# Performance work log

Measured on AMD Instinct MI355X. Metric: run time of the kernel, lower is better.

## Reference

```python
import jax, jax.numpy as jnp
import numpy as np

NUM_HEADS = 12


def setup_inputs() -> dict:
    key = jax.random.key(0)
    k1, k2, k3, k4, k5 = jax.random.split(key, 5)
    B, N, C = 64, 197, 768
    P = 10  # prefix length
    H, D = NUM_HEADS, C // NUM_HEADS
    return {
        "x": jax.random.normal(k1, (B, N, C), dtype=jnp.float32),
        "prompt": jax.random.normal(k2, (B, 2, P, H, D), dtype=jnp.float32),
        "qkv_w": jax.random.normal(k3, (3 * C, C), dtype=jnp.float32) * 0.02,
        "proj_w": jax.random.normal(k4, (C, C), dtype=jnp.float32) * 0.02,
        "proj_b": jax.random.normal(k5, (C,), dtype=jnp.float32) * 0.02,
    }


def reference(x, prompt, qkv_w, proj_w, proj_b):
    B, N, C = x.shape
    H = NUM_HEADS
    D = C // H
    scale = D ** -0.5

    # qkv projection (no bias), split into per-head q, k, v: [B, H, N, D]
    qkv = jnp.einsum("bnc,fc->bnf", x, qkv_w)              # [B, N, 3C]
    qkv = qkv.reshape(B, N, 3, H, D).transpose(2, 0, 3, 1, 4)
    q, k, v = qkv[0], qkv[1], qkv[2]

    # prompt: [B, 2, P, H, D] -> [2, B, H, P, D]; concat prefix onto k, v
    p = prompt.transpose(1, 0, 3, 2, 4)
    k = jnp.concatenate([p[0], k], axis=2)                  # [B, H, P+N, D]
    v = jnp.concatenate([p[1], v], axis=2)

    attn = jnp.einsum("bhnd,bhmd->bhnm", q, k) * scale      # [B, H, N, P+N]
    attn = jax.nn.softmax(attn, axis=-1)                    # attn_drop p=0 -> identity

    out = jnp.einsum("bhnm,bhmd->bhnd", attn, v)            # [B, H, N, D]
    out = out.transpose(0, 2, 1, 3).reshape(B, N, C)
    out = jnp.einsum("bnc,oc->bno", out, proj_w) + proj_b   # proj_drop p=0 -> identity
    return out
```

## Files before the change

### kernel.cpp

```cpp
#include <hip/hip_runtime.h>
#include <hip/hip_bf16.h>
#include <stdint.h>

#define NH 12
#define DH 64
#define CC 768
#define NTOK 197
#define PFX 10
#define MKV 207
#define BB 64
#define MROWS (BB * NTOK)
#define MPAD (99 * 128)
#define NT_QKV 9
#define MT_QKV 50
#define MPAD2 (MT_QKV * 256)
#define KV_PAD 208
#define KV_PAD2 224

typedef __attribute__((__ext_vector_type__(8))) short bf16x8;
typedef __attribute__((__ext_vector_type__(4))) float f32x4;

__device__ __forceinline__ ushort f2bf(float f) {
    union { float f; uint32_t u; } x; x.f = f;
    uint32_t u = x.u;
    return (ushort)((u + 0x7fffu + ((u >> 16) & 1u)) >> 16);
}

__device__ __forceinline__ void gload_lds16(const void* g, void* l) {
    __builtin_amdgcn_global_load_lds(
        (const __attribute__((address_space(1))) void*)g,
        (__attribute__((address_space(3))) void*)l, 16, 0, 0);
}

__device__ __forceinline__ int xcd_chunked(int orig, int nwg) {
    int q = nwg >> 3, r = nwg & 7;
    int xcd = orig & 7, rem = orig >> 3;
    return (xcd < r ? xcd * (q + 1) : r * (q + 1) + (xcd - r) * q) + rem;
}

__global__ void cvt_bf16(const float* __restrict__ src, ushort* __restrict__ dst, int n4) {
    int i = blockIdx.x * 256 + threadIdx.x;
    if (i >= n4) return;
    float4 v = reinterpret_cast<const float4*>(src)[i];
    ushort4 o = make_ushort4(f2bf(v.x), f2bf(v.y), f2bf(v.z), f2bf(v.w));
    reinterpret_cast<ushort4*>(dst)[i] = o;
}

__global__ void prompt_scatter(const float* __restrict__ prompt,
                               ushort* __restrict__ kbuf, ushort* __restrict__ vt) {
    int i = blockIdx.x * 256 + threadIdx.x;
    if (i >= BB * 2 * PFX * NH * DH) return;
    int d = i & 63;
    int h = (i >> 6) % NH;
    int p = (i / (64 * NH)) % PFX;
    int s = (i / (64 * NH * PFX)) & 1;
    int b = i / (64 * NH * PFX * 2);
    ushort val = f2bf(prompt[i]);
    int bh = b * NH + h;
    if (s == 0) kbuf[(bh * KV_PAD + p) * DH + d] = val;
    else        vt[(bh * DH + d) * KV_PAD2 + p] = val;
}


#define STAGE6(kt) {                                                              \
    const int bsel = (kt) & 1; const int koff = (kt) * 64;                        \
    gload_lds16(pA[0] + koff, &lds[bsel][0][0 * 4096 + w * 512]);                 \
    gload_lds16(pA[2] + koff, &lds[bsel][0][2 * 4096 + w * 512]);                 \
    gload_lds16(pB[0] + koff, &lds[bsel][1][0 * 4096 + w * 512]);                 \
    gload_lds16(pB[1] + koff, &lds[bsel][1][1 * 4096 + w * 512]);                 \
    gload_lds16(pB[2] + koff, &lds[bsel][1][2 * 4096 + w * 512]);                 \
    gload_lds16(pB[3] + koff, &lds[bsel][1][3 * 4096 + w * 512]); }

#define STAGE2(kt) {                                                              \
    const int bsel = (kt) & 1; const int koff = (kt) * 64;                        \
    gload_lds16(pA[1] + koff, &lds[bsel][0][1 * 4096 + w * 512]);                 \
    gload_lds16(pA[3] + koff, &lds[bsel][0][3 * 4096 + w * 512]); }

#define PHASE(t, p, VMSTR, DOSTAGE) {                                             \
    if (DOSTAGE) { if ((p) == 0) STAGE6((t) + 1) else STAGE2((t) + 1) }           \
    asm volatile("s_waitcnt vmcnt(" VMSTR ")" ::: "memory");                      \
    __builtin_amdgcn_s_barrier();                                                 \
    __builtin_amdgcn_sched_barrier(0);                                            \
    const ushort* Ab = &lds[(t) & 1][0][0];                                       \
    const ushort* Bb = &lds[(t) & 1][1][0];                                       \
    bf16x8 af[4][2], bf[4][2];                                                    \
    _Pragma("unroll") for (int i = 0; i < 4; ++i)                                 \
      _Pragma("unroll") for (int ks = 0; ks < 2; ++ks)                            \
        af[i][ks] = *reinterpret_cast<const bf16x8*>(                             \
            &Ab[(wm * 128 + ((p) * 4 + i) * 16 + lr) * 64 + coff[ks]]);           \
    _Pragma("unroll") for (int n = 0; n < 4; ++n)                                 \
      _Pragma("unroll") for (int ks = 0; ks < 2; ++ks)                            \
        bf[n][ks] = *reinterpret_cast<const bf16x8*>(                             \
            &Bb[(wn * 64 + n * 16 + lr) * 64 + coff[ks]]);                        \
    __builtin_amdgcn_s_setprio(1);                                                \
    _Pragma("unroll") for (int ks = 0; ks < 2; ++ks)                              \
      _Pragma("unroll") for (int i = 0; i < 4; ++i)                               \
        _Pragma("unroll") for (int n = 0; n < 4; ++n)                             \
          acc[(p) * 4 + i][n] = __builtin_amdgcn_mfma_f32_16x16x32_bf16(          \
              af[i][ks], bf[n][ks], acc[(p) * 4 + i][n], 0, 0, 0);                \
    __builtin_amdgcn_s_setprio(0);                                                \
    __builtin_amdgcn_s_barrier();                                                 \
    __builtin_amdgcn_sched_barrier(0);                                            \
}

__global__ __launch_bounds__(512, 2) void gemm_qkv8(const ushort* __restrict__ A,
                                                    const ushort* __restrict__ Bw,
                                                    ushort* __restrict__ qbuf,
                                                    ushort* __restrict__ kbuf,
                                                    ushort* __restrict__ vt) {
    __shared__ __align__(16) ushort lds[2][2][256 * 64];
    const int tid  = threadIdx.x;
    const int lane = tid & 63;
    const int w    = tid >> 6;
    const int wm = w >> 2, wn = w & 3;
    const int g = lane >> 4, lr = lane & 15;
    const int wgid = xcd_chunked(blockIdx.x, gridDim.x);
    const int row0 = (wgid / NT_QKV) * 256;
    const int col0 = (wgid % NT_QKV) * 256;

    const int sr  = tid >> 3;
    const int scb = (((tid & 7) ^ ((tid >> 3) & 7)) << 3);
    const int lr7 = lr & 7;
    int coff[2];
    coff[0] = ((0 * 4 + g) ^ lr7) << 3;
    coff[1] = ((1 * 4 + g) ^ lr7) << 3;

    const ushort* pA[4];
    #pragma unroll
    for (int q = 0; q < 4; ++q)
        pA[q] = A + (size_t)(row0 + q * 64 + sr) * CC + scb;
    const ushort* pB[4];
    #pragma unroll
    for (int j = 0; j < 4; ++j)
        pB[j] = Bw + (size_t)(col0 + j * 64 + sr) * CC + scb;

    f32x4 acc[8][4] = {};

    STAGE6(0)
    STAGE2(0)

    for (int t = 0; t < 11; ++t) {
        PHASE(t, 0, "8", true)
        PHASE(t, 1, "8", true)
    }
    PHASE(11, 0, "2", false)
    PHASE(11, 1, "0", false)

    #pragma unroll
    for (int ni = 0; ni < 4; ++ni) {
        int f = col0 + wn * 64 + ni * 16 + lr;
        int s   = f / CC;
        int rem = f - s * CC;
        int h = rem >> 6, d = rem & 63;
        #pragma unroll
        for (int mi = 0; mi < 8; ++mi) {
            #pragma unroll
            for (int rr = 0; rr < 4; ++rr) {
                int r = row0 + wm * 128 + mi * 16 + g * 4 + rr;
                if (r >= MROWS) continue;
                int b = r / NTOK;
                int n = r - b * NTOK;
                ushort val = f2bf(acc[mi][ni][rr]);
                int bh = b * NH + h;
                if (s == 0)      qbuf[(bh * KV_PAD + n) * DH + d] = val;
                else if (s == 1) kbuf[(bh * KV_PAD + n + PFX) * DH + d] = val;
                else             vt[(bh * DH + d) * KV_PAD2 + n + PFX] = val;
            }
        }
    }
}

#define GEMM_PRE(A_, B_, KDIM, NTILES)                                               \
    __shared__ __align__(16) ushort Alds0[128 * 32];                                 \
    __shared__ __align__(16) ushort Blds0[128 * 32];                                 \
    __shared__ __align__(16) ushort Alds1[128 * 32];                                 \
    __shared__ __align__(16) ushort Blds1[128 * 32];                                 \
    const int tid  = threadIdx.x;                                                    \
    const int lane = tid & 63;                                                       \
    const int wave = tid >> 6;                                                       \
    const int wm = wave >> 1, wn = wave & 1;                                         \
    const int g = lane >> 4, lr = lane & 15;                                         \
    const int wgid = xcd_chunked(blockIdx.x, gridDim.x);                             \
    const int row0 = (wgid / (NTILES)) * 128;                                        \
    const int col0 = (wgid % (NTILES)) * 128;                                        \
    const int srow = lane >> 2;                                                      \
    const int scol = (lane & 3) * 8;                                                 \
    const ushort* gA0 = &(A_)[(size_t)(row0 + wave * 16 + srow) * (KDIM) + scol];    \
    const ushort* gA1 = gA0 + (size_t)64 * (KDIM);                                   \
    const ushort* gB0 = &(B_)[(size_t)(col0 + wave * 16 + srow) * (KDIM) + scol];    \
    const ushort* gB1 = gB0 + (size_t)64 * (KDIM);                                   \
    f32x4 acc[4][4] = {};

#define GEMM_STAGE(AB, BB_, KOFF)                                                    \
    gload_lds16(gA0 + (KOFF), &(AB)[(wave * 16) * 32]);                              \
    gload_lds16(gA1 + (KOFF), &(AB)[(64 + wave * 16) * 32]);                         \
    gload_lds16(gB0 + (KOFF), &(BB_)[(wave * 16) * 32]);                             \
    gload_lds16(gB1 + (KOFF), &(BB_)[(64 + wave * 16) * 32]);

#define GEMM_COMPUTE(AB, BB_)                                                        \
    {                                                                                \
        bf16x8 af[4], bfr[4];                                                        \
        _Pragma("unroll")                                                            \
        for (int i = 0; i < 4; ++i)                                                  \
            af[i] = *reinterpret_cast<const bf16x8*>(&(AB)[(wm * 64 + i * 16 + lr) * 32 + g * 8]); \
        _Pragma("unroll")                                                            \
        for (int i = 0; i < 4; ++i)                                                  \
            bfr[i] = *reinterpret_cast<const bf16x8*>(&(BB_)[(wn * 64 + i * 16 + lr) * 32 + g * 8]); \
        _Pragma("unroll")                                                            \
        for (int mi = 0; mi < 4; ++mi)                                               \
            _Pragma("unroll")                                                        \
            for (int ni = 0; ni < 4; ++ni)                                           \
                acc[mi][ni] = __builtin_amdgcn_mfma_f32_16x16x32_bf16(af[mi], bfr[ni], acc[mi][ni], 0, 0, 0); \
    }

#define GEMM_MAIN(A_, B_, KDIM, NTILES)                                              \
    GEMM_PRE(A_, B_, KDIM, NTILES)                                                   \
    GEMM_STAGE(Alds0, Blds0, 0)                                                      \
    __syncthreads();                                                                 \
    for (int k0 = 0; k0 < (KDIM); k0 += 64) {                                        \
        GEMM_STAGE(Alds1, Blds1, k0 + 32)                                            \
        GEMM_COMPUTE(Alds0, Blds0)                                                   \
        __syncthreads();                                                             \
        if (k0 + 64 < (KDIM)) { GEMM_STAGE(Alds0, Blds0, k0 + 64) }                  \
        GEMM_COMPUTE(Alds1, Blds1)                                                   \
        __syncthreads();                                                             \
    }

__global__ __launch_bounds__(256) void gemm_proj(const ushort* __restrict__ A,
                                                 const ushort* __restrict__ Bw,
                                                 const float* __restrict__ bias,
                                                 float* __restrict__ out) {
    GEMM_MAIN(A, Bw, CC, 6)
    #pragma unroll
    for (int ni = 0; ni < 4; ++ni) {
        int o = col0 + wn * 64 + ni * 16 + lr;
        float bs = bias[o];
        #pragma unroll
        for (int mi = 0; mi < 4; ++mi) {
            #pragma unroll
            for (int rr = 0; rr < 4; ++rr) {
                int r = row0 + wm * 64 + mi * 16 + g * 4 + rr;
                if (r >= MROWS) continue;
                out[(size_t)r * CC + o] = acc[mi][ni][rr] + bs;
            }
        }
    }
}

__global__ __launch_bounds__(64) void attn(const ushort* __restrict__ qbuf,
                                           const ushort* __restrict__ kbuf,
                                           const ushort* __restrict__ vt,
                                           ushort* __restrict__ aout) {
    __shared__ __align__(16) ushort Plds[16][232];
    const int lane = threadIdx.x;
    const int g = lane >> 4, lr = lane & 15;
    const int wgid = xcd_chunked(blockIdx.x, gridDim.x);
    const int bh = wgid / 13;
    const int qt = wgid % 13;
    const int b = bh / NH;
    const int h = bh - b * NH;
    const ushort* Q  = qbuf + (size_t)bh * KV_PAD * DH;
    const ushort* Kb = kbuf + (size_t)bh * KV_PAD * DH;
    const ushort* V  = vt   + (size_t)bh * DH * KV_PAD2;

    bf16x8 qf[2];
    #pragma unroll
    for (int kc = 0; kc < 2; ++kc)
        qf[kc] = *reinterpret_cast<const bf16x8*>(&Q[(qt * 16 + lr) * DH + kc * 32 + g * 8]);

    f32x4 s[13];
    __builtin_amdgcn_s_setprio(1);
    #pragma unroll
    for (int t = 0; t < 13; ++t) {
        f32x4 a = {};
        #pragma unroll
        for (int kc = 0; kc < 2; ++kc) {
            bf16x8 kf = *reinterpret_cast<const bf16x8*>(&Kb[(t * 16 + lr) * DH + kc * 32 + g * 8]);
            a = __builtin_amdgcn_mfma_f32_16x16x32_bf16(kf, qf[kc], a, 0, 0, 0);
        }
        s[t] = a;
    }
    __builtin_amdgcn_s_setprio(0);

    float m = -1e30f;
    #pragma unroll
    for (int t = 0; t < 13; ++t) {
        #pragma unroll
        for (int rr = 0; rr < 4; ++rr) {
            int kv = t * 16 + g * 4 + rr;
            float v = (kv < MKV) ? s[t][rr] : -1e30f;
            s[t][rr] = v;
            m = fmaxf(m, v);
        }
    }
    m = fmaxf(m, __shfl_xor(m, 16));
    m = fmaxf(m, __shfl_xor(m, 32));

    const float cs = 0.125f * 1.4426950408889634f;
    float sum = 0.f;
    #pragma unroll
    for (int t = 0; t < 13; ++t) {
        #pragma unroll
        for (int rr = 0; rr < 4; ++rr) {
            float p = exp2f((s[t][rr] - m) * cs);
            s[t][rr] = p;
            sum += p;
        }
    }
    sum += __shfl_xor(sum, 16);
    sum += __shfl_xor(sum, 32);
    float inv = 1.0f / sum;

    {
        int row = lane >> 2;
        int col = 208 + (lane & 3) * 4;
        *reinterpret_cast<ushort4*>(&Plds[row][col]) = make_ushort4(0, 0, 0, 0);
    }
    #pragma unroll
    for (int t = 0; t < 13; ++t) {
        #pragma unroll
        for (int rr = 0; rr < 4; ++rr)
            Plds[lr][t * 16 + g * 4 + rr] = f2bf(s[t][rr] * inv);
    }
    __syncthreads();

    const int q = qt * 16 + lr;
    #pragma unroll
    for (int dt = 0; dt < 4; ++dt) {
        f32x4 o = {};
        __builtin_amdgcn_s_setprio(1);
        #pragma unroll
        for (int kc = 0; kc < 7; ++kc) {
            bf16x8 vf = *reinterpret_cast<const bf16x8*>(&V[(dt * 16 + lr) * KV_PAD2 + kc * 32 + g * 8]);
            bf16x8 pf = *reinterpret_cast<const bf16x8*>(&Plds[lr][kc * 32 + g * 8]);
            o = __builtin_amdgcn_mfma_f32_16x16x32_bf16(vf, pf, o, 0, 0, 0);
        }
        __builtin_amdgcn_s_setprio(0);
        if (q < NTOK) {
            ushort4 st = make_ushort4(f2bf(o[0]), f2bf(o[1]), f2bf(o[2]), f2bf(o[3]));
            int r = b * NTOK + q;
            *reinterpret_cast<ushort4*>(&aout[(size_t)r * CC + h * 64 + dt * 16 + g * 4]) = st;
        }
    }
}

extern "C" void kernel_launch(void* const* d_in, const int* in_sizes, int n_in,
                              void* d_out, int out_size, void* d_ws, size_t ws_size,
                              hipStream_t stream) {
    const float* x      = (const float*)d_in[0];
    const float* prompt = (const float*)d_in[1];
    const float* qkv_w  = (const float*)d_in[2];
    const float* proj_w = (const float*)d_in[3];
    const float* proj_b = (const float*)d_in[4];
    float* out = (float*)d_out;

    char* ws = (char*)d_ws;
    ushort* Xb = (ushort*)(ws + 0);
    ushort* Wq = (ushort*)(ws + 19660800);
    ushort* Wp = (ushort*)(ws + 23199744);
    ushort* qb = (ushort*)(ws + 24379392);
    ushort* kb = (ushort*)(ws + 44826624);
    ushort* vt = (ushort*)(ws + 65273856);
    ushort* ao = (ushort*)(ws + 87293952);

    cvt_bf16<<<dim3((MROWS * CC / 4 + 255) / 256), 256, 0, stream>>>(x, Xb, MROWS * CC / 4);
    cvt_bf16<<<dim3((3 * CC * CC / 4 + 255) / 256), 256, 0, stream>>>(qkv_w, Wq, 3 * CC * CC / 4);
    cvt_bf16<<<dim3((CC * CC / 4 + 255) / 256), 256, 0, stream>>>(proj_w, Wp, CC * CC / 4);
    prompt_scatter<<<dim3((BB * 2 * PFX * NH * DH + 255) / 256), 256, 0, stream>>>(prompt, kb, vt);

    gemm_qkv8<<<dim3(MT_QKV * NT_QKV), 512, 0, stream>>>(Xb, Wq, qb, kb, vt);
    attn<<<dim3(13 * BB * NH), 64, 0, stream>>>(qb, kb, vt, ao);
    gemm_proj<<<dim3(99 * 6), 256, 0, stream>>>(ao, Wp, proj_b, out);
}
```

Baseline: 298.2 us.

## Process all query tiles of a head per block with K/V staged in LDS

Replaces the per-query-tile attention kernel with one workgroup per (batch, head) whose eight waves share K and V loaded once into LDS (K with an XOR swizzle, V with a padded stride). This removes the 13-fold redundant global/L2 reads of K and V across query tiles. Large LDS use limits occupancy, and waves 0-4 process two query tiles while others process one, creating imbalance.

```diff
diff --git a/kernel.cpp b/kernel.cpp
--- a/kernel.cpp
+++ b/kernel.cpp
@@ -16,6 +16,7 @@
 #define MPAD2 (MT_QKV * 256)
 #define KV_PAD 208
 #define KV_PAD2 224
+#define VSTRIDE 232
 
 typedef __attribute__((__ext_vector_type__(8))) short bf16x8;
 typedef __attribute__((__ext_vector_type__(4))) float f32x4;
@@ -60,7 +61,6 @@
     if (s == 0) kbuf[(bh * KV_PAD + p) * DH + d] = val;
     else        vt[(bh * DH + d) * KV_PAD2 + p] = val;
 }
-
 
 #define STAGE6(kt) {                                                              \
     const int bsel = (kt) & 1; const int koff = (kt) * 64;                        \
@@ -247,101 +247,135 @@
     }
 }
 
-__global__ __launch_bounds__(64) void attn(const ushort* __restrict__ qbuf,
-                                           const ushort* __restrict__ kbuf,
-                                           const ushort* __restrict__ vt,
-                                           ushort* __restrict__ aout) {
-    __shared__ __align__(16) ushort Plds[16][232];
-    const int lane = threadIdx.x;
+__global__ __launch_bounds__(512, 2) void attn_bh(const ushort* __restrict__ qbuf,
+                                                  const ushort* __restrict__ kbuf,
+                                                  const ushort* __restrict__ vt,
+                                                  ushort* __restrict__ aout) {
+    __shared__ __align__(16) ushort Klds[KV_PAD * DH];
+    __shared__ __align__(16) ushort Vlds[DH * VSTRIDE];
+    __shared__ __align__(16) ushort Plds[8 * 16 * VSTRIDE];
+    const int tid  = threadIdx.x;
+    const int lane = tid & 63;
+    const int w    = tid >> 6;
     const int g = lane >> 4, lr = lane & 15;
-    const int wgid = xcd_chunked(blockIdx.x, gridDim.x);
-    const int bh = wgid / 13;
-    const int qt = wgid % 13;
-    const int b = bh / NH;
-    const int h = bh - b * NH;
-    const ushort* Q  = qbuf + (size_t)bh * KV_PAD * DH;
-    const ushort* Kb = kbuf + (size_t)bh * KV_PAD * DH;
-    const ushort* V  = vt   + (size_t)bh * DH * KV_PAD2;
-
-    bf16x8 qf[2];
+    const int bh = blockIdx.x;
+    const int b = bh / NH, h = bh - b * NH;
+
+    const ushort* pKsrc = kbuf + (size_t)bh * KV_PAD * DH
+                        + (lane >> 3) * DH + (((lane & 7) ^ (lane >> 3)) << 3);
+    #pragma unroll
+    for (int u = 0; u < 4; ++u) {
+        int uu = w + u * 8;
+        if (uu < 26) gload_lds16(pKsrc + uu * 512, &Klds[uu * 512]);
+    }
+
+    const int4* vsrc = reinterpret_cast<const int4*>(vt + (size_t)bh * DH * KV_PAD2);
+    #pragma unroll
+    for (int k = 0; k < 4; ++k) {
+        int u = tid + 512 * k;
+        if (u < DH * (KV_PAD2 / 8)) {
+            int4 d = vsrc[u];
+            int row  = u / (KV_PAD2 / 8);
+            int colu = u - row * (KV_PAD2 / 8);
+            *reinterpret_cast<int4*>(&Vlds[row * VSTRIDE + colu * 8]) = d;
+        }
+    }
+
+    const ushort* Q = qbuf + (size_t)bh * KV_PAD * DH;
+    const int qt0 = w, qt1 = w + 8;
+    bf16x8 qf0[2], qf1[2];
     #pragma unroll
     for (int kc = 0; kc < 2; ++kc)
-        qf[kc] = *reinterpret_cast<const bf16x8*>(&Q[(qt * 16 + lr) * DH + kc * 32 + g * 8]);
-
-    f32x4 s[13];
-    __builtin_amdgcn_s_setprio(1);
-    #pragma unroll
-    for (int t = 0; t < 13; ++t) {
-        f32x4 a = {};
-        #pragma unroll
-        for (int kc = 0; kc < 2; ++kc) {
-            bf16x8 kf = *reinterpret_cast<const bf16x8*>(&Kb[(t * 16 + lr) * DH + kc * 32 + g * 8]);
-            a = __builtin_amdgcn_mfma_f32_16x16x32_bf16(kf, qf[kc], a, 0, 0, 0);
-        }
-        s[t] = a;
-    }
-    __builtin_amdgcn_s_setprio(0);
-
-    float m = -1e30f;
-    #pragma unroll
-    for (int t = 0; t < 13; ++t) {
-        #pragma unroll
-        for (int rr = 0; rr < 4; ++rr) {
-            int kv = t * 16 + g * 4 + rr;
-            float v = (kv < MKV) ? s[t][rr] : -1e30f;
-            s[t][rr] = v;
-            m = fmaxf(m, v);
-        }
-    }
-    m = fmaxf(m, __shfl_xor(m, 16));
-    m = fmaxf(m, __shfl_xor(m, 32));
-
+        qf0[kc] = *reinterpret_cast<const bf16x8*>(&Q[(qt0 * 16 + lr) * DH + kc * 32 + g * 8]);
+    if (qt1 < 13) {
+        #pragma unroll
+        for (int kc = 0; kc < 2; ++kc)
+            qf1[kc] = *reinterpret_cast<const bf16x8*>(&Q[(qt1 * 16 + lr) * DH + kc * 32 + g * 8]);
+    }
+
+    __syncthreads();
+
+    ushort* Pw = &Plds[w * 16 * VSTRIDE];
+    {
+        int row = lane >> 2, col = 208 + (lane & 3) * 4;
+        *reinterpret_cast<ushort4*>(&Pw[row * VSTRIDE + col]) = make_ushort4(0, 0, 0, 0);
+    }
+
+    const int kswz0 = ((0 * 4 + g) ^ (lr & 7)) << 3;
+    const int kswz1 = ((1 * 4 + g) ^ (lr & 7)) << 3;
     const float cs = 0.125f * 1.4426950408889634f;
-    float sum = 0.f;
-    #pragma unroll
-    for (int t = 0; t < 13; ++t) {
-        #pragma unroll
-        for (int rr = 0; rr < 4; ++rr) {
-            float p = exp2f((s[t][rr] - m) * cs);
-            s[t][rr] = p;
-            sum += p;
-        }
-    }
-    sum += __shfl_xor(sum, 16);
-    sum += __shfl_xor(sum, 32);
-    float inv = 1.0f / sum;
-
-    {
-        int row = lane >> 2;
-        int col = 208 + (lane & 3) * 4;
-        *reinterpret_cast<ushort4*>(&Plds[row][col]) = make_ushort4(0, 0, 0, 0);
-    }
-    #pragma unroll
-    for (int t = 0; t < 13; ++t) {
-        #pragma unroll
-        for (int rr = 0; rr < 4; ++rr)
-            Plds[lr][t * 16 + g * 4 + rr] = f2bf(s[t][rr] * inv);
-    }
-    __syncthreads();
-
-    const int q = qt * 16 + lr;
-    #pragma unroll
-    for (int dt = 0; dt < 4; ++dt) {
-        f32x4 o = {};
+
+    auto process = [&](int qt, bf16x8 qfa, bf16x8 qfb) {
+        f32x4 s[13];
         __builtin_amdgcn_s_setprio(1);
         #pragma unroll
-        for (int kc = 0; kc < 7; ++kc) {
-            bf16x8 vf = *reinterpret_cast<const bf16x8*>(&V[(dt * 16 + lr) * KV_PAD2 + kc * 32 + g * 8]);
-            bf16x8 pf = *reinterpret_cast<const bf16x8*>(&Plds[lr][kc * 32 + g * 8]);
-            o = __builtin_amdgcn_mfma_f32_16x16x32_bf16(vf, pf, o, 0, 0, 0);
+        for (int t = 0; t < 13; ++t) {
+            f32x4 a = {};
+            bf16x8 kf0 = *reinterpret_cast<const bf16x8*>(&Klds[(t * 16 + lr) * DH + kswz0]);
+            a = __builtin_amdgcn_mfma_f32_16x16x32_bf16(kf0, qfa, a, 0, 0, 0);
+            bf16x8 kf1 = *reinterpret_cast<const bf16x8*>(&Klds[(t * 16 + lr) * DH + kswz1]);
+            a = __builtin_amdgcn_mfma_f32_16x16x32_bf16(kf1, qfb, a, 0, 0, 0);
+            s[t] = a;
         }
         __builtin_amdgcn_s_setprio(0);
-        if (q < NTOK) {
-            ushort4 st = make_ushort4(f2bf(o[0]), f2bf(o[1]), f2bf(o[2]), f2bf(o[3]));
-            int r = b * NTOK + q;
-            *reinterpret_cast<ushort4*>(&aout[(size_t)r * CC + h * 64 + dt * 16 + g * 4]) = st;
-        }
-    }
+
+        float m = -1e30f;
+        #pragma unroll
+        for (int t = 0; t < 13; ++t) {
+            #pragma unroll
+            for (int rr = 0; rr < 4; ++rr) {
+                int kv = t * 16 + g * 4 + rr;
+                float v = (kv < MKV) ? s[t][rr] : -1e30f;
+                s[t][rr] = v;
+                m = fmaxf(m, v);
+            }
+        }
+        m = fmaxf(m, __shfl_xor(m, 16));
+        m = fmaxf(m, __shfl_xor(m, 32));
+
+        float sum = 0.f;
+        #pragma unroll
+        for (int t = 0; t < 13; ++t) {
+            #pragma unroll
+            for (int rr = 0; rr < 4; ++rr) {
+                float p = exp2f((s[t][rr] - m) * cs);
+                s[t][rr] = p;
+                sum += p;
+            }
+        }
+        sum += __shfl_xor(sum, 16);
+        sum += __shfl_xor(sum, 32);
+        float inv = 1.0f / sum;
+
+        #pragma unroll
+        for (int t = 0; t < 13; ++t) {
+            #pragma unroll
+            for (int rr = 0; rr < 4; ++rr)
+                Pw[lr * VSTRIDE + t * 16 + g * 4 + rr] = f2bf(s[t][rr] * inv);
+        }
+
+        const int q = qt * 16 + lr;
+        #pragma unroll
+        for (int dt = 0; dt < 4; ++dt) {
+            f32x4 o = {};
+            __builtin_amdgcn_s_setprio(1);
+            #pragma unroll
+            for (int kc = 0; kc < 7; ++kc) {
+                bf16x8 vf = *reinterpret_cast<const bf16x8*>(&Vlds[(dt * 16 + lr) * VSTRIDE + kc * 32 + g * 8]);
+                bf16x8 pf = *reinterpret_cast<const bf16x8*>(&Pw[lr * VSTRIDE + kc * 32 + g * 8]);
+                o = __builtin_amdgcn_mfma_f32_16x16x32_bf16(vf, pf, o, 0, 0, 0);
+            }
+            __builtin_amdgcn_s_setprio(0);
+            if (q < NTOK) {
+                ushort4 st = make_ushort4(f2bf(o[0]), f2bf(o[1]), f2bf(o[2]), f2bf(o[3]));
+                int r = b * NTOK + q;
+                *reinterpret_cast<ushort4*>(&aout[(size_t)r * CC + h * 64 + dt * 16 + g * 4]) = st;
+            }
+        }
+    };
+
+    process(qt0, qf0[0], qf0[1]);
+    if (qt1 < 13) process(qt1, qf1[0], qf1[1]);
 }
 
 extern "C" void kernel_launch(void* const* d_in, const int* in_sizes, int n_in,
@@ -369,6 +403,6 @@
     prompt_scatter<<<dim3((BB * 2 * PFX * NH * DH + 255) / 256), 256, 0, stream>>>(prompt, kb, vt);
 
     gemm_qkv8<<<dim3(MT_QKV * NT_QKV), 512, 0, stream>>>(Xb, Wq, qb, kb, vt);
-    attn<<<dim3(13 * BB * NH), 64, 0, stream>>>(qb, kb, vt, ao);
+    attn_bh<<<dim3(BB * NH), 512, 0, stream>>>(qb, kb, vt, ao);
     gemm_proj<<<dim3(99 * 6), 256, 0, stream>>>(ao, Wp, proj_b, out);
 }
```

Result: faster. 278.3 us (-6.7%).
